# Kernel tuning notes

Hardware: AMD Instinct MI355X
Metric: run time of the kernel (lower is better)

## Reference

```python
import jax, jax.numpy as jnp
import numpy as np

N_NODES = 100000
N_EDGES = 3200000
N_GRAPHS = 2000
F_IN, H, N_CLS = 14, 64, 2


def _glorot(key, shape):
    lim = float(np.sqrt(6.0 / (shape[0] + shape[1])))
    return jax.random.uniform(key, shape, jnp.float32, -lim, lim)


def setup_inputs() -> dict:
    key = jax.random.key(0)
    ks = jax.random.split(key, 16)
    x = jax.random.normal(ks[0], (N_NODES, F_IN), jnp.float32)
    edge_index = jax.random.randint(ks[1], (2, N_EDGES), 0, N_NODES, jnp.int64)
    batch = jnp.sort(jax.random.randint(ks[2], (N_NODES,), 0, N_GRAPHS, jnp.int64))
    return {
        "x": x,
        "W1l": _glorot(ks[3], (F_IN, H)), "W1r": _glorot(ks[4], (F_IN, H)), "b1": jnp.zeros((H,), jnp.float32),
        "W2l": _glorot(ks[5], (H, H)), "W2r": _glorot(ks[6], (H, H)), "b2": jnp.zeros((H,), jnp.float32),
        "W3l": _glorot(ks[7], (H, H)), "W3r": _glorot(ks[8], (H, H)), "b3": jnp.zeros((H,), jnp.float32),
        "W4l": _glorot(ks[9], (H, N_CLS)), "W4r": _glorot(ks[10], (H, N_CLS)), "b4": jnp.zeros((N_CLS,), jnp.float32),
        "edge_index": edge_index,
        "batch": batch,
    }


def _sage_conv(x, Wl, Wr, b, src, dst, inv_deg):
    # mean-aggregate neighbor features: messages flow src -> dst (PyG SAGEConv default)
    agg = jax.ops.segment_sum(x[src], dst, num_segments=N_NODES) * inv_deg
    return agg @ Wl + x @ Wr + b


def reference(x, W1l, W1r, b1, W2l, W2r, b2, W3l, W3r, b3, W4l, W4r, b4, edge_index, batch):
    src, dst = edge_index[0], edge_index[1]
    ones = jnp.ones((src.shape[0],), x.dtype)
    deg = jax.ops.segment_sum(ones, dst, num_segments=N_NODES)
    inv_deg = (1.0 / jnp.maximum(deg, 1.0))[:, None]  # [N,1], isolated nodes -> 0 agg

    h = jax.nn.relu(_sage_conv(x, W1l, W1r, b1, src, dst, inv_deg))
    h = jax.nn.relu(_sage_conv(h, W2l, W2r, b2, src, dst, inv_deg))
    h = jax.nn.relu(_sage_conv(h, W3l, W3r, b3, src, dst, inv_deg))
    h = _sage_conv(h, W4l, W4r, b4, src, dst, inv_deg)

    # global_mean_pool over graphs
    gsum = jax.ops.segment_sum(h, batch, num_segments=N_GRAPHS)
    gcnt = jax.ops.segment_sum(jnp.ones((h.shape[0],), h.dtype), batch, num_segments=N_GRAPHS)
    pooled = gsum / jnp.maximum(gcnt, 1.0)[:, None]
    return jax.nn.log_softmax(pooled, axis=-1)
```

## Files before the change

### kernel.cpp

```cpp
#include <hip/hip_runtime.h>
#include <hip/hip_fp16.h>

#define NN 100000
#define NE 3200000
#define NG 2000
#define FIN 14
#define HD 64
#define NC 2

#define NBUK 256
#define BNODES 391
#define P1E 4096
#define BUFCAP 13312

typedef unsigned int uint;
typedef short short8 __attribute__((ext_vector_type(8)));
typedef float f32x4 __attribute__((ext_vector_type(4)));
union U128 { uint4 u; short8 s; };

__device__ __forceinline__ __half2 u2h(uint u) {
    union { uint u; __half2 h; } c; c.u = u; return c.h;
}
__device__ __forceinline__ uint h2u(__half2 h) {
    union { __half2 h; uint u; } c; c.h = h; return c.u;
}
__device__ __forceinline__ uint pkh(float a, float b) {
    return h2u(__floats2half2_rn(a, b));
}
__device__ __forceinline__ uint pack2bf16(float a, float b) {
    uint ua = __float_as_uint(a), ub = __float_as_uint(b);
    ua = (ua + 0x7FFFu + ((ua >> 16) & 1u)) >> 16;
    ub = (ub + 0x7FFFu + ((ub >> 16) & 1u)) >> 16;
    return ua | (ub << 16);
}
__device__ __forceinline__ short bf16of(float a) {
    uint ua = __float_as_uint(a);
    return (short)((ua + 0x7FFFu + ((ua >> 16) & 1u)) >> 16);
}


__global__ __launch_bounds__(256) void k_hist_bucket(const int* __restrict__ dst,
                                                     int* __restrict__ bkcnt) {
    __shared__ int cnt[NBUK];
    int t = threadIdx.x;
    cnt[t] = 0;
    __syncthreads();
    int e0 = blockIdx.x * P1E;
    int m = NE - e0; if (m > P1E) m = P1E;
    for (int e = t; e < m; e += 256) atomicAdd(&cnt[dst[e0 + e] / BNODES], 1);
    __syncthreads();
    if (cnt[t] > 0) atomicAdd(&bkcnt[t], cnt[t]);
}

__global__ void k_scanb(const int* __restrict__ bkcnt, int* __restrict__ bbase,
                        int* __restrict__ bcur) {
    __shared__ int tmp[NBUK];
    int t = threadIdx.x;
    int v = bkcnt[t];
    tmp[t] = v;
    __syncthreads();
    for (int off = 1; off < NBUK; off <<= 1) {
        int u = (t >= off) ? tmp[t - off] : 0;
        __syncthreads();
        tmp[t] += u;
        __syncthreads();
    }
    int excl = tmp[t] - v;
    bbase[t] = excl;
    bcur[t] = excl;
    if (t == NBUK - 1) bbase[NBUK] = tmp[t];
}

__global__ void k_gbounds(const int* __restrict__ batch, int* __restrict__ gstart,
                          int* __restrict__ gend) {
    int i = blockIdx.x * blockDim.x + threadIdx.x;
    if (i < NN) {
        int b = batch[i];
        if (i == 0 || batch[i - 1] != b) gstart[b] = i;
        if (i == NN - 1 || batch[i + 1] != b) gend[b] = i + 1;
    }
}

__global__ __launch_bounds__(256) void k_pass1(
    const int* __restrict__ src, const int* __restrict__ dst,
    int* __restrict__ bcur, int* __restrict__ pairs) {
    __shared__ int cnt[NBUK];
    __shared__ int scanb[NBUK + 1];
    __shared__ int cur[NBUK];
    __shared__ int gbase[NBUK];
    __shared__ int pbuf[P1E];
    __shared__ unsigned char bsl[P1E];
    int t = threadIdx.x;
    int e0 = blockIdx.x * P1E;
    int m = NE - e0; if (m > P1E) m = P1E;
    cnt[t] = 0;
    __syncthreads();
    int ds[16], ss[16], bk[16];
#pragma unroll
    for (int j = 0; j < 16; ++j) {
        int e = t + j * 256;
        if (e < m) {
            ds[j] = dst[e0 + e];
            ss[j] = src[e0 + e];
            bk[j] = ds[j] / BNODES;
            atomicAdd(&cnt[bk[j]], 1);
        } else bk[j] = -1;
    }
    __syncthreads();
    int v = cnt[t];
    scanb[t] = v;
    __syncthreads();
    for (int off = 1; off < 256; off <<= 1) {
        int u = (t >= off) ? scanb[t - off] : 0;
        __syncthreads();
        scanb[t] += u;
        __syncthreads();
    }
    int excl = scanb[t] - v;
    scanb[t] = excl;
    cur[t] = excl;
    if (t == 255) scanb[256] = excl + v;
    __syncthreads();
#pragma unroll
    for (int j = 0; j < 16; ++j) {
        if (bk[j] >= 0) {
            int p = atomicAdd(&cur[bk[j]], 1);
            pbuf[p] = ss[j] | ((ds[j] - bk[j] * BNODES) << 17);
            bsl[p] = (unsigned char)bk[j];
        }
    }
    int cb = scanb[t + 1] - scanb[t];
    if (cb > 0) gbase[t] = atomicAdd(&bcur[t], cb);
    __syncthreads();
    for (int s = t; s < m; s += 256) {
        int b = bsl[s];
        pairs[gbase[b] + (s - scanb[b])] = pbuf[s];
    }
}

__global__ __launch_bounds__(256) void k_pass2(
    const int* __restrict__ pairs, const int* __restrict__ bbase,
    int* __restrict__ deg, int* __restrict__ rs, int* __restrict__ csr) {
    __shared__ int buf1[BUFCAP];
    __shared__ int buf2[BUFCAP];
    __shared__ int cnt[512];
    __shared__ int rsl[512];
    __shared__ int cur[512];
    __shared__ int s1[256];
    int b = blockIdx.x;
    int n0 = b * BNODES;
    if (n0 >= NN) return;
    int nlocal = NN - n0; if (nlocal > BNODES) nlocal = BNODES;
    int t = threadIdx.x;
    int base = bbase[b];
    int m = bbase[b + 1] - base;
    bool fits = (m <= BUFCAP);
    cnt[t] = 0; cnt[t + 256] = 0;
    __syncthreads();
    for (int s = t; s < m; s += 256) {
        int pk = pairs[base + s];
        if (fits) buf1[s] = pk;
        atomicAdd(&cnt[(uint)pk >> 17], 1);
    }
    __syncthreads();
    int c0 = cnt[2 * t], c1 = cnt[2 * t + 1];
    int ps = c0 + c1;
    s1[t] = ps;
    __syncthreads();
    for (int off = 1; off < 256; off <<= 1) {
        int u = (t >= off) ? s1[t - off] : 0;
        __syncthreads();
        s1[t] += u;
        __syncthreads();
    }
    int pexcl = s1[t] - ps;
    rsl[2 * t] = pexcl;          cur[2 * t] = pexcl;
    rsl[2 * t + 1] = pexcl + c0; cur[2 * t + 1] = pexcl + c0;
    __syncthreads();
    for (int i = t; i < nlocal; i += 256) {
        deg[n0 + i] = cnt[i];
        rs[n0 + i] = base + rsl[i];
    }
    if (fits) {
        for (int s = t; s < m; s += 256) {
            int pk = buf1[s];
            int p = atomicAdd(&cur[(uint)pk >> 17], 1);
            buf2[p] = pk & 0x1FFFF;
        }
        __syncthreads();
        for (int s = t; s < m; s += 256) csr[base + s] = buf2[s];
    } else {
        for (int s = t; s < m; s += 256) {
            int pk = pairs[base + s];
            int p = atomicAdd(&cur[(uint)pk >> 17], 1);
            csr[base + p] = pk & 0x1FFFF;
        }
    }
}


__global__ void k_packx(const float* __restrict__ x, uint* __restrict__ xh) {
    int t = blockIdx.x * blockDim.x + threadIdx.x;
    if (t < NN * 8) {
        int row = t >> 3, q = t & 7;
        int j0 = 2 * q, j1 = 2 * q + 1;
        float f0 = (j0 < FIN) ? x[row * FIN + j0] : 0.f;
        float f1 = (j1 < FIN) ? x[row * FIN + j1] : 0.f;
        xh[t] = pkh(f0, f1);
    }
}


__global__ __launch_bounds__(256, 6) void k_layer1(
    const float* __restrict__ x, const uint* __restrict__ xh, uint* __restrict__ hout,
    const float* __restrict__ Wl, const float* __restrict__ Wr, const float* __restrict__ b,
    const int* __restrict__ rs, const int* __restrict__ deg, const int* __restrict__ csr) {
    __shared__ float2 sW[FIN][HD];
    __shared__ float sb[HD];
    __shared__ float2 sAH[4][16];
    for (int i = threadIdx.x; i < FIN * HD; i += 256) {
        int k = i >> 6, j = i & 63;
        sW[k][j] = make_float2(Wl[i], Wr[i]);
    }
    if (threadIdx.x < HD) sb[threadIdx.x] = b[threadIdx.x];
    __syncthreads();
    int lane = threadIdx.x & 63, wid = threadIdx.x >> 6;
    int sub = lane >> 3;
    int fq = lane & 7;
    int ngroups = (NN + 3) / 4;
    for (int g = blockIdx.x; g < ngroups; g += gridDim.x) {
        int n = g * 4 + wid;
        bool act = n < NN;
        if (act) {
            int s0 = rs[n], d = deg[n];
            float xv = (lane < FIN) ? x[n * FIN + lane] : 0.f;
            __half2 Z = __float2half2_rn(0.f);
            __half2 A0 = Z, A1 = Z, A2 = Z, A3 = Z, A4 = Z, A5 = Z, A6 = Z, A7 = Z;
            for (int base = 0; base < d; base += 64) {
                int rem = d - base; if (rem > 64) rem = 64;
                int idxv = (lane < rem) ? csr[s0 + base + lane] : 0;
                int j = 0;
                for (; j + 64 <= rem; j += 64) {
                    int i0 = __shfl(idxv, j + 0 + sub);
                    int i1 = __shfl(idxv, j + 8 + sub);
                    int i2 = __shfl(idxv, j + 16 + sub);
                    int i3 = __shfl(idxv, j + 24 + sub);
                    int i4 = __shfl(idxv, j + 32 + sub);
                    int i5 = __shfl(idxv, j + 40 + sub);
                    int i6 = __shfl(idxv, j + 48 + sub);
                    int i7 = __shfl(idxv, j + 56 + sub);
                    A0 = __hadd2(A0, u2h(xh[(size_t)i0 * 8 + fq]));
                    A1 = __hadd2(A1, u2h(xh[(size_t)i1 * 8 + fq]));
                    A2 = __hadd2(A2, u2h(xh[(size_t)i2 * 8 + fq]));
                    A3 = __hadd2(A3, u2h(xh[(size_t)i3 * 8 + fq]));
                    A4 = __hadd2(A4, u2h(xh[(size_t)i4 * 8 + fq]));
                    A5 = __hadd2(A5, u2h(xh[(size_t)i5 * 8 + fq]));
                    A6 = __hadd2(A6, u2h(xh[(size_t)i6 * 8 + fq]));
                    A7 = __hadd2(A7, u2h(xh[(size_t)i7 * 8 + fq]));
                }
                for (; j + 8 <= rem; j += 8) {
                    int i0 = __shfl(idxv, j + sub);
                    A0 = __hadd2(A0, u2h(xh[(size_t)i0 * 8 + fq]));
                }
                if (j < rem) {
                    int i0 = __shfl(idxv, j + sub);
                    if (sub < rem - j) A0 = __hadd2(A0, u2h(xh[(size_t)i0 * 8 + fq]));
                }
            }
            A0 = __hadd2(A0, A1); A2 = __hadd2(A2, A3);
            A4 = __hadd2(A4, A5); A6 = __hadd2(A6, A7);
            A0 = __hadd2(A0, A2); A4 = __hadd2(A4, A6);
            A0 = __hadd2(A0, A4);
            float ax = __low2float(A0), ay = __high2float(A0);
            for (int off = 8; off <= 32; off <<= 1) {
                ax += __shfl_xor(ax, off);
                ay += __shfl_xor(ay, off);
            }
            float inv = 1.0f / (float)(d > 1 ? d : 1);
            float e0 = __shfl(ax, lane >> 1);
            float e1 = __shfl(ay, lane >> 1);
            float sel = (lane & 1) ? e1 : e0;
            if (lane < 16) sAH[wid][lane] = make_float2((lane < FIN) ? sel * inv : 0.f, xv);
        }
        float out = sb[lane];
#pragma unroll
        for (int k = 0; k < FIN; ++k) {
            float2 w = sW[k][lane];
            float2 ah = sAH[wid][k];
            out += ah.x * w.x + ah.y * w.y;
        }
        out = fmaxf(out, 0.f);
        float o2 = __shfl_xor(out, 1);
        if (act && !(lane & 1)) hout[(size_t)n * 32 + (lane >> 1)] = pkh(out, o2);
    }
}


template <bool FUSEZ>
__global__ __launch_bounds__(256, 4) void k_layerH(
    const uint* __restrict__ hin, uint* __restrict__ hout,
    const float* __restrict__ Wl, const float* __restrict__ Wr, const float* __restrict__ b,
    const float* __restrict__ W4l, float* __restrict__ z,
    const int* __restrict__ rs, const int* __restrict__ deg, const int* __restrict__ csr) {
    __shared__ uint AH[16 * 64];
    __shared__ float zb[4][16][2];
    int lane = threadIdx.x & 63, wid = threadIdx.x >> 6;
    int r16 = lane & 15, qg = lane >> 4;
    int jj = 16 * wid + r16;
    short8 bfr[4];
#pragma unroll
    for (int c = 0; c < 4; ++c) {
#pragma unroll
        for (int i = 0; i < 8; ++i) {
            int k = 32 * c + 8 * qg + i;
            float v = (k < 64) ? Wl[k * 64 + jj] : Wr[(k - 64) * 64 + jj];
            bfr[c][i] = bf16of(v);
        }
    }
    float bv = b[jj];
    float wz0 = 0.f, wz1 = 0.f;
    if (FUSEZ) { wz0 = W4l[jj * NC + 0]; wz1 = W4l[jj * NC + 1]; }
    int sub = lane >> 4;
    int fq = lane & 15;
    const uint2* hb2 = (const uint2*)hin;
    int n0 = blockIdx.x * 16;
    for (int i = 0; i < 4; ++i) {
        int irow = wid * 4 + i;
        int n = n0 + irow;
        int swz = (irow & 7) << 2;
        if (n < NN) {
            int s0 = rs[n], d = deg[n];
            __half2 Zh = __float2half2_rn(0.f);
            __half2 P0 = Zh, P1 = Zh, P2 = Zh, P3 = Zh, P4 = Zh, P5 = Zh, P6 = Zh, P7 = Zh;
            __half2 Q0 = Zh, Q1 = Zh, Q2 = Zh, Q3 = Zh, Q4 = Zh, Q5 = Zh, Q6 = Zh, Q7 = Zh;
            for (int base = 0; base < d; base += 64) {
                int rem = d - base; if (rem > 64) rem = 64;
                int idxv = (lane < rem) ? csr[s0 + base + lane] : 0;
                int j = 0;
                for (; j + 32 <= rem; j += 32) {
                    int i0 = __shfl(idxv, j + 0 + sub);
                    int i1 = __shfl(idxv, j + 4 + sub);
                    int i2 = __shfl(idxv, j + 8 + sub);
                    int i3 = __shfl(idxv, j + 12 + sub);
                    int i4 = __shfl(idxv, j + 16 + sub);
                    int i5 = __shfl(idxv, j + 20 + sub);
                    int i6 = __shfl(idxv, j + 24 + sub);
                    int i7 = __shfl(idxv, j + 28 + sub);
                    uint2 U;
                    U = hb2[(size_t)i0 * 16 + fq]; P0 = __hadd2(P0, u2h(U.x)); Q0 = __hadd2(Q0, u2h(U.y));
                    U = hb2[(size_t)i1 * 16 + fq]; P1 = __hadd2(P1, u2h(U.x)); Q1 = __hadd2(Q1, u2h(U.y));
                    U = hb2[(size_t)i2 * 16 + fq]; P2 = __hadd2(P2, u2h(U.x)); Q2 = __hadd2(Q2, u2h(U.y));
                    U = hb2[(size_t)i3 * 16 + fq]; P3 = __hadd2(P3, u2h(U.x)); Q3 = __hadd2(Q3, u2h(U.y));
                    U = hb2[(size_t)i4 * 16 + fq]; P4 = __hadd2(P4, u2h(U.x)); Q4 = __hadd2(Q4, u2h(U.y));
                    U = hb2[(size_t)i5 * 16 + fq]; P5 = __hadd2(P5, u2h(U.x)); Q5 = __hadd2(Q5, u2h(U.y));
                    U = hb2[(size_t)i6 * 16 + fq]; P6 = __hadd2(P6, u2h(U.x)); Q6 = __hadd2(Q6, u2h(U.y));
                    U = hb2[(size_t)i7 * 16 + fq]; P7 = __hadd2(P7, u2h(U.x)); Q7 = __hadd2(Q7, u2h(U.y));
                }
                for (; j + 4 <= rem; j += 4) {
                    int i0 = __shfl(idxv, j + sub);
                    uint2 U = hb2[(size_t)i0 * 16 + fq];
                    P0 = __hadd2(P0, u2h(U.x)); Q0 = __hadd2(Q0, u2h(U.y));
                }
                if (j < rem) {
                    int i0 = __shfl(idxv, j + sub);
                    if (sub < rem - j) {
                        uint2 U = hb2[(size_t)i0 * 16 + fq];
                        P0 = __hadd2(P0, u2h(U.x)); Q0 = __hadd2(Q0, u2h(U.y));
                    }
                }
            }
            P0 = __hadd2(P0, P1); P2 = __hadd2(P2, P3);
            P4 = __hadd2(P4, P5); P6 = __hadd2(P6, P7);
            Q0 = __hadd2(Q0, Q1); Q2 = __hadd2(Q2, Q3);
            Q4 = __hadd2(Q4, Q5); Q6 = __hadd2(Q6, Q7);
            P0 = __hadd2(P0, P2); P4 = __hadd2(P4, P6);
            Q0 = __hadd2(Q0, Q2); Q4 = __hadd2(Q4, Q6);
            P0 = __hadd2(P0, P4); Q0 = __hadd2(Q0, Q4);
            float ax = __low2float(P0), ay = __high2float(P0);
            float az = __low2float(Q0), aw = __high2float(Q0);
            for (int off = 16; off <= 32; off <<= 1) {
                ax += __shfl_xor(ax, off);
                ay += __shfl_xor(ay, off);
                az += __shfl_xor(az, off);
                aw += __shfl_xor(aw, off);
            }
            float inv = 1.0f / (float)(d > 1 ? d : 1);
            ax *= inv; ay *= inv; az *= inv; aw *= inv;
            if (lane < 16) {
                uint2* p = (uint2*)&AH[irow * 64 + ((2 * fq) ^ swz)];
                *p = make_uint2(pack2bf16(ax, ay), pack2bf16(az, aw));
            }
            if (lane < 32) {
                __half2 hh = u2h(hin[(size_t)n * 32 + lane]);
                AH[irow * 64 + ((32 + lane) ^ swz)] = pack2bf16(__low2float(hh), __high2float(hh));
            }
        } else {
            AH[irow * 64 + lane] = 0;
        }
    }
    __syncthreads();
    f32x4 acc = (f32x4){bv, bv, bv, bv};
#pragma unroll
    for (int c = 0; c < 4; ++c) {
        U128 a;
        a.u = *(const uint4*)&AH[r16 * 64 + ((16 * c + 4 * qg) ^ ((r16 & 7) << 2))];
        acc = __builtin_amdgcn_mfma_f32_16x16x32_bf16(a.s, bfr[c], acc, 0, 0, 0);
    }
    float rz0[4], rz1[4];
#pragma unroll
    for (int r = 0; r < 4; ++r) {
        int m = n0 + qg * 4 + r;
        float out = fmaxf(acc[r], 0.f);
        float o2 = __shfl_xor(out, 1);
        if (!(lane & 1) && m < NN)
            hout[(size_t)m * 32 + 8 * wid + (r16 >> 1)] = pkh(out, o2);
        if (FUSEZ) { rz0[r] = out * wz0; rz1[r] = out * wz1; }
    }
    if (FUSEZ) {
#pragma unroll
        for (int r = 0; r < 4; ++r) {
            float a0 = rz0[r], a1 = rz1[r];
            for (int off = 1; off < 16; off <<= 1) {
                a0 += __shfl_xor(a0, off);
                a1 += __shfl_xor(a1, off);
            }
            if (r16 == 0) { zb[wid][qg * 4 + r][0] = a0; zb[wid][qg * 4 + r][1] = a1; }
        }
        __syncthreads();
        int t = threadIdx.x;
        if (t < 16 && n0 + t < NN) {
            float a0 = zb[0][t][0] + zb[1][t][0] + zb[2][t][0] + zb[3][t][0];
            float a1 = zb[0][t][1] + zb[1][t][1] + zb[2][t][1] + zb[3][t][1];
            ((float2*)z)[n0 + t] = make_float2(a0, a1);
        }
    }
}


__global__ __launch_bounds__(256) void k_pool(
    const uint* __restrict__ h3, const float* __restrict__ z,
    const float* __restrict__ W4r, const float* __restrict__ b4,
    const int* __restrict__ rs, const int* __restrict__ deg, const int* __restrict__ csr,
    const int* __restrict__ batch, float* __restrict__ gsum) {
    __shared__ float sW[HD * NC];
    if (threadIdx.x < HD * NC) sW[threadIdx.x] = W4r[threadIdx.x];
    __syncthreads();
    const float2* z2 = (const float2*)z;
    int lane = threadIdx.x & 63, wid = threadIdx.x >> 6;
    int stride = gridDim.x * 4;
    for (int n = blockIdx.x * 4 + wid; n < NN; n += stride) {
        float r0 = 0.f, r1 = 0.f;
        if (lane < 32) {
            __half2 h = u2h(h3[(size_t)n * 32 + lane]);
            float f0 = __low2float(h), f1 = __high2float(h);
            r0 = f0 * sW[(2 * lane) * NC + 0] + f1 * sW[(2 * lane + 1) * NC + 0];
            r1 = f0 * sW[(2 * lane) * NC + 1] + f1 * sW[(2 * lane + 1) * NC + 1];
        }
        int s0 = rs[n], d = deg[n];
        float a0 = 0.f, a1 = 0.f;
        for (int j = lane; j < d; j += 64) {
            int s = csr[s0 + j];
            float2 zv = z2[s];
            a0 += zv.x;
            a1 += zv.y;
        }
        for (int off = 32; off; off >>= 1) {
            r0 += __shfl_xor(r0, off);
            r1 += __shfl_xor(r1, off);
            a0 += __shfl_xor(a0, off);
            a1 += __shfl_xor(a1, off);
        }
        if (lane == 0) {
            float inv = 1.0f / (float)(d > 1 ? d : 1);
            float o0 = a0 * inv + r0 + b4[0];
            float o1 = a1 * inv + r1 + b4[1];
            int gg = batch[n];
            atomicAdd(&gsum[gg * 2 + 0], o0);
            atomicAdd(&gsum[gg * 2 + 1], o1);
        }
    }
}

__global__ void k_final(const float* __restrict__ gsum, const int* __restrict__ gstart,
                        const int* __restrict__ gend, float* __restrict__ out) {
    int g = blockIdx.x * blockDim.x + threadIdx.x;
    if (g < NG) {
        int cnt = gend[g] - gstart[g];
        float inv = 1.0f / (float)(cnt > 1 ? cnt : 1);
        float p0 = gsum[g * 2 + 0] * inv;
        float p1 = gsum[g * 2 + 1] * inv;
        float m = fmaxf(p0, p1);
        float lse = m + logf(expf(p0 - m) + expf(p1 - m));
        out[g * 2 + 0] = p0 - lse;
        out[g * 2 + 1] = p1 - lse;
    }
}


extern "C" void kernel_launch(void* const* d_in, const int* in_sizes, int n_in,
                              void* d_out, int out_size, void* d_ws, size_t ws_size,
                              hipStream_t stream) {
    const float* x   = (const float*)d_in[0];
    const float* W1l = (const float*)d_in[1];
    const float* W1r = (const float*)d_in[2];
    const float* b1  = (const float*)d_in[3];
    const float* W2l = (const float*)d_in[4];
    const float* W2r = (const float*)d_in[5];
    const float* b2  = (const float*)d_in[6];
    const float* W3l = (const float*)d_in[7];
    const float* W3r = (const float*)d_in[8];
    const float* b3  = (const float*)d_in[9];
    const float* W4l = (const float*)d_in[10];
    const float* W4r = (const float*)d_in[11];
    const float* b4  = (const float*)d_in[12];
    const int* ei    = (const int*)d_in[13];
    const int* batch = (const int*)d_in[14];
    const int* src = ei;
    const int* dst = ei + NE;
    float* out = (float*)d_out;

    char* w = (char*)d_ws;
    int* deg    = (int*)w; w += (size_t)NN * 4;
    int* rs     = (int*)w; w += (size_t)NN * 4;
    int* csr    = (int*)w; w += (size_t)NE * 4;
    int* gstart = (int*)w; w += (size_t)NG * 4;
    int* gend   = (int*)w; w += (size_t)NG * 4;
    int* bkcnt  = (int*)w; w += NBUK * 4;
    int* bbase  = (int*)w; w += (NBUK + 1) * 4;
    int* bcur   = (int*)w; w += NBUK * 4;
    w = (char*)(((uintptr_t)w + 255) & ~(uintptr_t)255);
    uint* xh    = (uint*)w; w += (size_t)NN * 8 * 4;
    uint* hA    = (uint*)w; w += (size_t)NN * 32 * 4;
    uint* hB    = (uint*)w; w += (size_t)NN * 32 * 4;
    float* z    = (float*)w; w += (size_t)NN * NC * 4;
    float* gsum = (float*)w; w += (size_t)NG * NC * 4;
    int* pairs = (int*)hB;

    const int P1B = (NE + P1E - 1) / P1E;
    const int HGB = (NN + 15) / 16;

    hipMemsetAsync(bkcnt, 0, NBUK * 4, stream);
    hipMemsetAsync(gstart, 0, (size_t)NG * 4, stream);
    hipMemsetAsync(gend, 0, (size_t)NG * 4, stream);
    hipMemsetAsync(gsum, 0, (size_t)NG * NC * 4, stream);

    k_hist_bucket<<<P1B, 256, 0, stream>>>(dst, bkcnt);
    k_packx<<<(NN * 8 + 255) / 256, 256, 0, stream>>>(x, xh);
    k_gbounds<<<(NN + 255) / 256, 256, 0, stream>>>(batch, gstart, gend);
    k_scanb<<<1, NBUK, 0, stream>>>(bkcnt, bbase, bcur);
    k_pass1<<<P1B, 256, 0, stream>>>(src, dst, bcur, pairs);
    k_pass2<<<NBUK, 256, 0, stream>>>(pairs, bbase, deg, rs, csr);

    k_layer1<<<1536, 256, 0, stream>>>(x, xh, hA, W1l, W1r, b1, rs, deg, csr);
    k_layerH<false><<<HGB, 256, 0, stream>>>(hA, hB, W2l, W2r, b2, nullptr, nullptr, rs, deg, csr);
    k_layerH<true><<<HGB, 256, 0, stream>>>(hB, hA, W3l, W3r, b3, W4l, z, rs, deg, csr);
    k_pool<<<2048, 256, 0, stream>>>(hA, z, W4r, b4, rs, deg, csr, batch, gsum);
    k_final<<<(NG + 255) / 256, 256, 0, stream>>>(gsum, gstart, gend, out);
}
```

Baseline: 424.3 us.

## Load CSR indices directly per lane, reduce in half2, fuse root projection into layer3

```diff
diff --git a/kernel.cpp b/kernel.cpp
--- a/kernel.cpp
+++ b/kernel.cpp
@@ -36,6 +36,9 @@
 __device__ __forceinline__ short bf16of(float a) {
     uint ua = __float_as_uint(a);
     return (short)((ua + 0x7FFFu + ((ua >> 16) & 1u)) >> 16);
+}
+__device__ __forceinline__ __half2 hredx(__half2 v, int off) {
+    return __hadd2(v, u2h((uint)__shfl_xor((int)h2u(v), off)));
 }
 
 
@@ -225,57 +228,53 @@
     if (threadIdx.x < HD) sb[threadIdx.x] = b[threadIdx.x];
     __syncthreads();
     int lane = threadIdx.x & 63, wid = threadIdx.x >> 6;
-    int sub = lane >> 3;
-    int fq = lane & 7;
+    int sub8 = lane >> 3;
+    int fq8 = lane & 7;
     int ngroups = (NN + 3) / 4;
     for (int g = blockIdx.x; g < ngroups; g += gridDim.x) {
         int n = g * 4 + wid;
         bool act = n < NN;
         if (act) {
             int s0 = rs[n], d = deg[n];
+            const int* cp = csr + s0;
             float xv = (lane < FIN) ? x[n * FIN + lane] : 0.f;
             __half2 Z = __float2half2_rn(0.f);
             __half2 A0 = Z, A1 = Z, A2 = Z, A3 = Z, A4 = Z, A5 = Z, A6 = Z, A7 = Z;
-            for (int base = 0; base < d; base += 64) {
-                int rem = d - base; if (rem > 64) rem = 64;
-                int idxv = (lane < rem) ? csr[s0 + base + lane] : 0;
-                int j = 0;
-                for (; j + 64 <= rem; j += 64) {
-                    int i0 = __shfl(idxv, j + 0 + sub);
-                    int i1 = __shfl(idxv, j + 8 + sub);
-                    int i2 = __shfl(idxv, j + 16 + sub);
-                    int i3 = __shfl(idxv, j + 24 + sub);
-                    int i4 = __shfl(idxv, j + 32 + sub);
-                    int i5 = __shfl(idxv, j + 40 + sub);
-                    int i6 = __shfl(idxv, j + 48 + sub);
-                    int i7 = __shfl(idxv, j + 56 + sub);
-                    A0 = __hadd2(A0, u2h(xh[(size_t)i0 * 8 + fq]));
-                    A1 = __hadd2(A1, u2h(xh[(size_t)i1 * 8 + fq]));
-                    A2 = __hadd2(A2, u2h(xh[(size_t)i2 * 8 + fq]));
-                    A3 = __hadd2(A3, u2h(xh[(size_t)i3 * 8 + fq]));
-                    A4 = __hadd2(A4, u2h(xh[(size_t)i4 * 8 + fq]));
-                    A5 = __hadd2(A5, u2h(xh[(size_t)i5 * 8 + fq]));
-                    A6 = __hadd2(A6, u2h(xh[(size_t)i6 * 8 + fq]));
-                    A7 = __hadd2(A7, u2h(xh[(size_t)i7 * 8 + fq]));
-                }
-                for (; j + 8 <= rem; j += 8) {
-                    int i0 = __shfl(idxv, j + sub);
-                    A0 = __hadd2(A0, u2h(xh[(size_t)i0 * 8 + fq]));
-                }
-                if (j < rem) {
-                    int i0 = __shfl(idxv, j + sub);
-                    if (sub < rem - j) A0 = __hadd2(A0, u2h(xh[(size_t)i0 * 8 + fq]));
-                }
+            int e = 0;
+            for (; e + 64 <= d; e += 64) {
+                int i0 = cp[e + 0 + sub8];
+                int i1 = cp[e + 8 + sub8];
+                int i2 = cp[e + 16 + sub8];
+                int i3 = cp[e + 24 + sub8];
+                int i4 = cp[e + 32 + sub8];
+                int i5 = cp[e + 40 + sub8];
+                int i6 = cp[e + 48 + sub8];
+                int i7 = cp[e + 56 + sub8];
+                A0 = __hadd2(A0, u2h(xh[(size_t)i0 * 8 + fq8]));
+                A1 = __hadd2(A1, u2h(xh[(size_t)i1 * 8 + fq8]));
+                A2 = __hadd2(A2, u2h(xh[(size_t)i2 * 8 + fq8]));
+                A3 = __hadd2(A3, u2h(xh[(size_t)i3 * 8 + fq8]));
+                A4 = __hadd2(A4, u2h(xh[(size_t)i4 * 8 + fq8]));
+                A5 = __hadd2(A5, u2h(xh[(size_t)i5 * 8 + fq8]));
+                A6 = __hadd2(A6, u2h(xh[(size_t)i6 * 8 + fq8]));
+                A7 = __hadd2(A7, u2h(xh[(size_t)i7 * 8 + fq8]));
+            }
+            for (; e + 8 <= d; e += 8) {
+                int i0 = cp[e + sub8];
+                A0 = __hadd2(A0, u2h(xh[(size_t)i0 * 8 + fq8]));
+            }
+            if (e < d) {
+                int ei = e + sub8;
+                int i0 = cp[ei < d ? ei : d - 1];
+                uint u = xh[(size_t)i0 * 8 + fq8];
+                if (ei < d) A0 = __hadd2(A0, u2h(u));
             }
             A0 = __hadd2(A0, A1); A2 = __hadd2(A2, A3);
             A4 = __hadd2(A4, A5); A6 = __hadd2(A6, A7);
             A0 = __hadd2(A0, A2); A4 = __hadd2(A4, A6);
             A0 = __hadd2(A0, A4);
+            A0 = hredx(A0, 8); A0 = hredx(A0, 16); A0 = hredx(A0, 32);
             float ax = __low2float(A0), ay = __high2float(A0);
-            for (int off = 8; off <= 32; off <<= 1) {
-                ax += __shfl_xor(ax, off);
-                ay += __shfl_xor(ay, off);
-            }
             float inv = 1.0f / (float)(d > 1 ? d : 1);
             float e0 = __shfl(ax, lane >> 1);
             float e1 = __shfl(ay, lane >> 1);
@@ -300,10 +299,11 @@
 __global__ __launch_bounds__(256, 4) void k_layerH(
     const uint* __restrict__ hin, uint* __restrict__ hout,
     const float* __restrict__ Wl, const float* __restrict__ Wr, const float* __restrict__ b,
-    const float* __restrict__ W4l, float* __restrict__ z,
+    const float* __restrict__ W4l, const float* __restrict__ W4r, const float* __restrict__ b4g,
+    float* __restrict__ z, float* __restrict__ s2,
     const int* __restrict__ rs, const int* __restrict__ deg, const int* __restrict__ csr) {
     __shared__ uint AH[16 * 64];
-    __shared__ float zb[4][16][2];
+    __shared__ float zb[4][16][4];
     int lane = threadIdx.x & 63, wid = threadIdx.x >> 6;
     int r16 = lane & 15, qg = lane >> 4;
     int jj = 16 * wid + r16;
@@ -318,9 +318,12 @@
         }
     }
     float bv = b[jj];
-    float wz0 = 0.f, wz1 = 0.f;
-    if (FUSEZ) { wz0 = W4l[jj * NC + 0]; wz1 = W4l[jj * NC + 1]; }
-    int sub = lane >> 4;
+    float wz0 = 0.f, wz1 = 0.f, ws0 = 0.f, ws1 = 0.f;
+    if (FUSEZ) {
+        wz0 = W4l[jj * NC + 0]; wz1 = W4l[jj * NC + 1];
+        ws0 = W4r[jj * NC + 0]; ws1 = W4r[jj * NC + 1];
+    }
+    int sub4 = lane >> 4;
     int fq = lane & 15;
     const uint2* hb2 = (const uint2*)hin;
     int n0 = blockIdx.x * 16;
@@ -330,44 +333,40 @@
         int swz = (irow & 7) << 2;
         if (n < NN) {
             int s0 = rs[n], d = deg[n];
+            const int* cp = csr + s0;
             __half2 Zh = __float2half2_rn(0.f);
             __half2 P0 = Zh, P1 = Zh, P2 = Zh, P3 = Zh, P4 = Zh, P5 = Zh, P6 = Zh, P7 = Zh;
             __half2 Q0 = Zh, Q1 = Zh, Q2 = Zh, Q3 = Zh, Q4 = Zh, Q5 = Zh, Q6 = Zh, Q7 = Zh;
-            for (int base = 0; base < d; base += 64) {
-                int rem = d - base; if (rem > 64) rem = 64;
-                int idxv = (lane < rem) ? csr[s0 + base + lane] : 0;
-                int j = 0;
-                for (; j + 32 <= rem; j += 32) {
-                    int i0 = __shfl(idxv, j + 0 + sub);
-                    int i1 = __shfl(idxv, j + 4 + sub);
-                    int i2 = __shfl(idxv, j + 8 + sub);
-                    int i3 = __shfl(idxv, j + 12 + sub);
-                    int i4 = __shfl(idxv, j + 16 + sub);
-                    int i5 = __shfl(idxv, j + 20 + sub);
-                    int i6 = __shfl(idxv, j + 24 + sub);
-                    int i7 = __shfl(idxv, j + 28 + sub);
-                    uint2 U;
-                    U = hb2[(size_t)i0 * 16 + fq]; P0 = __hadd2(P0, u2h(U.x)); Q0 = __hadd2(Q0, u2h(U.y));
-                    U = hb2[(size_t)i1 * 16 + fq]; P1 = __hadd2(P1, u2h(U.x)); Q1 = __hadd2(Q1, u2h(U.y));
-                    U = hb2[(size_t)i2 * 16 + fq]; P2 = __hadd2(P2, u2h(U.x)); Q2 = __hadd2(Q2, u2h(U.y));
-                    U = hb2[(size_t)i3 * 16 + fq]; P3 = __hadd2(P3, u2h(U.x)); Q3 = __hadd2(Q3, u2h(U.y));
-                    U = hb2[(size_t)i4 * 16 + fq]; P4 = __hadd2(P4, u2h(U.x)); Q4 = __hadd2(Q4, u2h(U.y));
-                    U = hb2[(size_t)i5 * 16 + fq]; P5 = __hadd2(P5, u2h(U.x)); Q5 = __hadd2(Q5, u2h(U.y));
-                    U = hb2[(size_t)i6 * 16 + fq]; P6 = __hadd2(P6, u2h(U.x)); Q6 = __hadd2(Q6, u2h(U.y));
-                    U = hb2[(size_t)i7 * 16 + fq]; P7 = __hadd2(P7, u2h(U.x)); Q7 = __hadd2(Q7, u2h(U.y));
-                }
-                for (; j + 4 <= rem; j += 4) {
-                    int i0 = __shfl(idxv, j + sub);
-                    uint2 U = hb2[(size_t)i0 * 16 + fq];
-                    P0 = __hadd2(P0, u2h(U.x)); Q0 = __hadd2(Q0, u2h(U.y));
-                }
-                if (j < rem) {
-                    int i0 = __shfl(idxv, j + sub);
-                    if (sub < rem - j) {
-                        uint2 U = hb2[(size_t)i0 * 16 + fq];
-                        P0 = __hadd2(P0, u2h(U.x)); Q0 = __hadd2(Q0, u2h(U.y));
-                    }
-                }
+            int e = 0;
+            for (; e + 32 <= d; e += 32) {
+                int i0 = cp[e + 0 + sub4];
+                int i1 = cp[e + 4 + sub4];
+                int i2 = cp[e + 8 + sub4];
+                int i3 = cp[e + 12 + sub4];
+                int i4 = cp[e + 16 + sub4];
+                int i5 = cp[e + 20 + sub4];
+                int i6 = cp[e + 24 + sub4];
+                int i7 = cp[e + 28 + sub4];
+                uint2 U;
+                U = hb2[(size_t)i0 * 16 + fq]; P0 = __hadd2(P0, u2h(U.x)); Q0 = __hadd2(Q0, u2h(U.y));
+                U = hb2[(size_t)i1 * 16 + fq]; P1 = __hadd2(P1, u2h(U.x)); Q1 = __hadd2(Q1, u2h(U.y));
+                U = hb2[(size_t)i2 * 16 + fq]; P2 = __hadd2(P2, u2h(U.x)); Q2 = __hadd2(Q2, u2h(U.y));
+                U = hb2[(size_t)i3 * 16 + fq]; P3 = __hadd2(P3, u2h(U.x)); Q3 = __hadd2(Q3, u2h(U.y));
+                U = hb2[(size_t)i4 * 16 + fq]; P4 = __hadd2(P4, u2h(U.x)); Q4 = __hadd2(Q4, u2h(U.y));
+                U = hb2[(size_t)i5 * 16 + fq]; P5 = __hadd2(P5, u2h(U.x)); Q5 = __hadd2(Q5, u2h(U.y));
+                U = hb2[(size_t)i6 * 16 + fq]; P6 = __hadd2(P6, u2h(U.x)); Q6 = __hadd2(Q6, u2h(U.y));
+                U = hb2[(size_t)i7 * 16 + fq]; P7 = __hadd2(P7, u2h(U.x)); Q7 = __hadd2(Q7, u2h(U.y));
+            }
+            for (; e + 4 <= d; e += 4) {
+                int i0 = cp[e + sub4];
+                uint2 U = hb2[(size_t)i0 * 16 + fq];
+                P0 = __hadd2(P0, u2h(U.x)); Q0 = __hadd2(Q0, u2h(U.y));
+            }
+            if (e < d) {
+                int ei = e + sub4;
+                int i0 = cp[ei < d ? ei : d - 1];
+                uint2 U = hb2[(size_t)i0 * 16 + fq];
+                if (ei < d) { P0 = __hadd2(P0, u2h(U.x)); Q0 = __hadd2(Q0, u2h(U.y)); }
             }
             P0 = __hadd2(P0, P1); P2 = __hadd2(P2, P3);
             P4 = __hadd2(P4, P5); P6 = __hadd2(P6, P7);
@@ -376,17 +375,12 @@
             P0 = __hadd2(P0, P2); P4 = __hadd2(P4, P6);
             Q0 = __hadd2(Q0, Q2); Q4 = __hadd2(Q4, Q6);
             P0 = __hadd2(P0, P4); Q0 = __hadd2(Q0, Q4);
-            float ax = __low2float(P0), ay = __high2float(P0);
-            float az = __low2float(Q0), aw = __high2float(Q0);
-            for (int off = 16; off <= 32; off <<= 1) {
-                ax += __shfl_xor(ax, off);
-                ay += __shfl_xor(ay, off);
-                az += __shfl_xor(az, off);
-                aw += __shfl_xor(aw, off);
-            }
+            P0 = hredx(P0, 16); P0 = hredx(P0, 32);
+            Q0 = hredx(Q0, 16); Q0 = hredx(Q0, 32);
             float inv = 1.0f / (float)(d > 1 ? d : 1);
-            ax *= inv; ay *= inv; az *= inv; aw *= inv;
             if (lane < 16) {
+                float ax = __low2float(P0) * inv, ay = __high2float(P0) * inv;
+                float az = __low2float(Q0) * inv, aw = __high2float(Q0) * inv;
                 uint2* p = (uint2*)&AH[irow * 64 + ((2 * fq) ^ swz)];
                 *p = make_uint2(pack2bf16(ax, ay), pack2bf16(az, aw));
             }
@@ -406,7 +400,7 @@
         a.u = *(const uint4*)&AH[r16 * 64 + ((16 * c + 4 * qg) ^ ((r16 & 7) << 2))];
         acc = __builtin_amdgcn_mfma_f32_16x16x32_bf16(a.s, bfr[c], acc, 0, 0, 0);
     }
-    float rz0[4], rz1[4];
+    float rz0[4], rz1[4], rs0[4], rs1[4];
 #pragma unroll
     for (int r = 0; r < 4; ++r) {
         int m = n0 + qg * 4 + r;
@@ -414,48 +408,49 @@
         float o2 = __shfl_xor(out, 1);
         if (!(lane & 1) && m < NN)
             hout[(size_t)m * 32 + 8 * wid + (r16 >> 1)] = pkh(out, o2);
-        if (FUSEZ) { rz0[r] = out * wz0; rz1[r] = out * wz1; }
+        if (FUSEZ) {
+            rz0[r] = out * wz0; rz1[r] = out * wz1;
+            rs0[r] = out * ws0; rs1[r] = out * ws1;
+        }
     }
     if (FUSEZ) {
 #pragma unroll
         for (int r = 0; r < 4; ++r) {
-            float a0 = rz0[r], a1 = rz1[r];
+            float a0 = rz0[r], a1 = rz1[r], b0 = rs0[r], b1 = rs1[r];
             for (int off = 1; off < 16; off <<= 1) {
                 a0 += __shfl_xor(a0, off);
                 a1 += __shfl_xor(a1, off);
-            }
-            if (r16 == 0) { zb[wid][qg * 4 + r][0] = a0; zb[wid][qg * 4 + r][1] = a1; }
+                b0 += __shfl_xor(b0, off);
+                b1 += __shfl_xor(b1, off);
+            }
+            if (r16 == 0) {
+                zb[wid][qg * 4 + r][0] = a0; zb[wid][qg * 4 + r][1] = a1;
+                zb[wid][qg * 4 + r][2] = b0; zb[wid][qg * 4 + r][3] = b1;
+            }
         }
         __syncthreads();
         int t = threadIdx.x;
         if (t < 16 && n0 + t < NN) {
             float a0 = zb[0][t][0] + zb[1][t][0] + zb[2][t][0] + zb[3][t][0];
             float a1 = zb[0][t][1] + zb[1][t][1] + zb[2][t][1] + zb[3][t][1];
+            float c0 = zb[0][t][2] + zb[1][t][2] + zb[2][t][2] + zb[3][t][2];
+            float c1 = zb[0][t][3] + zb[1][t][3] + zb[2][t][3] + zb[3][t][3];
             ((float2*)z)[n0 + t] = make_float2(a0, a1);
+            ((float2*)s2)[n0 + t] = make_float2(c0 + b4g[0], c1 + b4g[1]);
         }
     }
 }
 
 
 __global__ __launch_bounds__(256) void k_pool(
-    const uint* __restrict__ h3, const float* __restrict__ z,
-    const float* __restrict__ W4r, const float* __restrict__ b4,
+    const float* __restrict__ z, const float* __restrict__ s2,
     const int* __restrict__ rs, const int* __restrict__ deg, const int* __restrict__ csr,
     const int* __restrict__ batch, float* __restrict__ gsum) {
-    __shared__ float sW[HD * NC];
-    if (threadIdx.x < HD * NC) sW[threadIdx.x] = W4r[threadIdx.x];
-    __syncthreads();
     const float2* z2 = (const float2*)z;
+    const float2* s22 = (const float2*)s2;
     int lane = threadIdx.x & 63, wid = threadIdx.x >> 6;
     int stride = gridDim.x * 4;
     for (int n = blockIdx.x * 4 + wid; n < NN; n += stride) {
-        float r0 = 0.f, r1 = 0.f;
-        if (lane < 32) {
-            __half2 h = u2h(h3[(size_t)n * 32 + lane]);
-            float f0 = __low2float(h), f1 = __high2float(h);
-            r0 = f0 * sW[(2 * lane) * NC + 0] + f1 * sW[(2 * lane + 1) * NC + 0];
-            r1 = f0 * sW[(2 * lane) * NC + 1] + f1 * sW[(2 * lane + 1) * NC + 1];
-        }
         int s0 = rs[n], d = deg[n];
         float a0 = 0.f, a1 = 0.f;
         for (int j = lane; j < d; j += 64) {
@@ -465,15 +460,14 @@
             a1 += zv.y;
         }
         for (int off = 32; off; off >>= 1) {
-            r0 += __shfl_xor(r0, off);
-            r1 += __shfl_xor(r1, off);
             a0 += __shfl_xor(a0, off);
             a1 += __shfl_xor(a1, off);
         }
         if (lane == 0) {
+            float2 sv = s22[n];
             float inv = 1.0f / (float)(d > 1 ? d : 1);
-            float o0 = a0 * inv + r0 + b4[0];
-            float o1 = a1 * inv + r1 + b4[1];
+            float o0 = a0 * inv + sv.x;
+            float o1 = a1 * inv + sv.y;
             int gg = batch[n];
             atomicAdd(&gsum[gg * 2 + 0], o0);
             atomicAdd(&gsum[gg * 2 + 1], o1);
@@ -533,6 +527,7 @@
     uint* hA    = (uint*)w; w += (size_t)NN * 32 * 4;
     uint* hB    = (uint*)w; w += (size_t)NN * 32 * 4;
     float* z    = (float*)w; w += (size_t)NN * NC * 4;
+    float* s2   = (float*)w; w += (size_t)NN * NC * 4;
     float* gsum = (float*)w; w += (size_t)NG * NC * 4;
     int* pairs = (int*)hB;
 
@@ -552,8 +547,12 @@
     k_pass2<<<NBUK, 256, 0, stream>>>(pairs, bbase, deg, rs, csr);
 
     k_layer1<<<1536, 256, 0, stream>>>(x, xh, hA, W1l, W1r, b1, rs, deg, csr);
-    k_layerH<false><<<HGB, 256, 0, stream>>>(hA, hB, W2l, W2r, b2, nullptr, nullptr, rs, deg, csr);
-    k_layerH<true><<<HGB, 256, 0, stream>>>(hB, hA, W3l, W3r, b3, W4l, z, rs, deg, csr);
-    k_pool<<<2048, 256, 0, stream>>>(hA, z, W4r, b4, rs, deg, csr, batch, gsum);
+    k_layerH<false><<<HGB, 256, 0, stream>>>(hA, hB, W2l, W2r, b2,
+                                             nullptr, nullptr, nullptr, nullptr, nullptr,
+                                             rs, deg, csr);
+    k_layerH<true><<<HGB, 256, 0, stream>>>(hB, hA, W3l, W3r, b3,
+                                            W4l, W4r, b4, z, s2,
+                                            rs, deg, csr);
+    k_pool<<<2048, 256, 0, stream>>>(z, s2, rs, deg, csr, batch, gsum);
     k_final<<<(NG + 255) / 256, 256, 0, stream>>>(gsum, gstart, gend, out);
 }
```

After: 456.8 us. 1.08x slower.

## Fuse layer-4 root projection into layer-3 epilogue, halve shuffle reductions, raise occupancy

Applied to the files above, without the earlier changes.

```diff
diff --git a/kernel.cpp b/kernel.cpp
--- a/kernel.cpp
+++ b/kernel.cpp
@@ -36,6 +36,9 @@
 __device__ __forceinline__ short bf16of(float a) {
     uint ua = __float_as_uint(a);
     return (short)((ua + 0x7FFFu + ((ua >> 16) & 1u)) >> 16);
+}
+__device__ __forceinline__ __half2 hredx(__half2 v, int off) {
+    return __hadd2(v, u2h((uint)__shfl_xor((int)h2u(v), off)));
 }
 
 
@@ -271,11 +274,8 @@
             A4 = __hadd2(A4, A5); A6 = __hadd2(A6, A7);
             A0 = __hadd2(A0, A2); A4 = __hadd2(A4, A6);
             A0 = __hadd2(A0, A4);
+            A0 = hredx(A0, 8); A0 = hredx(A0, 16); A0 = hredx(A0, 32);
             float ax = __low2float(A0), ay = __high2float(A0);
-            for (int off = 8; off <= 32; off <<= 1) {
-                ax += __shfl_xor(ax, off);
-                ay += __shfl_xor(ay, off);
-            }
             float inv = 1.0f / (float)(d > 1 ? d : 1);
             float e0 = __shfl(ax, lane >> 1);
             float e1 = __shfl(ay, lane >> 1);
@@ -297,13 +297,14 @@
 
 
 template <bool FUSEZ>
-__global__ __launch_bounds__(256, 4) void k_layerH(
+__global__ __launch_bounds__(256, 8) void k_layerH(
     const uint* __restrict__ hin, uint* __restrict__ hout,
     const float* __restrict__ Wl, const float* __restrict__ Wr, const float* __restrict__ b,
-    const float* __restrict__ W4l, float* __restrict__ z,
+    const float* __restrict__ W4l, const float* __restrict__ W4r, const float* __restrict__ b4g,
+    float* __restrict__ z, float* __restrict__ s2,
     const int* __restrict__ rs, const int* __restrict__ deg, const int* __restrict__ csr) {
     __shared__ uint AH[16 * 64];
-    __shared__ float zb[4][16][2];
+    __shared__ float zb[4][16][4];
     int lane = threadIdx.x & 63, wid = threadIdx.x >> 6;
     int r16 = lane & 15, qg = lane >> 4;
     int jj = 16 * wid + r16;
@@ -318,8 +319,11 @@
         }
     }
     float bv = b[jj];
-    float wz0 = 0.f, wz1 = 0.f;
-    if (FUSEZ) { wz0 = W4l[jj * NC + 0]; wz1 = W4l[jj * NC + 1]; }
+    float wz0 = 0.f, wz1 = 0.f, ws0 = 0.f, ws1 = 0.f;
+    if (FUSEZ) {
+        wz0 = W4l[jj * NC + 0]; wz1 = W4l[jj * NC + 1];
+        ws0 = W4r[jj * NC + 0]; ws1 = W4r[jj * NC + 1];
+    }
     int sub = lane >> 4;
     int fq = lane & 15;
     const uint2* hb2 = (const uint2*)hin;
@@ -376,17 +380,12 @@
             P0 = __hadd2(P0, P2); P4 = __hadd2(P4, P6);
             Q0 = __hadd2(Q0, Q2); Q4 = __hadd2(Q4, Q6);
             P0 = __hadd2(P0, P4); Q0 = __hadd2(Q0, Q4);
-            float ax = __low2float(P0), ay = __high2float(P0);
-            float az = __low2float(Q0), aw = __high2float(Q0);
-            for (int off = 16; off <= 32; off <<= 1) {
-                ax += __shfl_xor(ax, off);
-                ay += __shfl_xor(ay, off);
-                az += __shfl_xor(az, off);
-                aw += __shfl_xor(aw, off);
-            }
+            P0 = hredx(P0, 16); P0 = hredx(P0, 32);
+            Q0 = hredx(Q0, 16); Q0 = hredx(Q0, 32);
             float inv = 1.0f / (float)(d > 1 ? d : 1);
-            ax *= inv; ay *= inv; az *= inv; aw *= inv;
             if (lane < 16) {
+                float ax = __low2float(P0) * inv, ay = __high2float(P0) * inv;
+                float az = __low2float(Q0) * inv, aw = __high2float(Q0) * inv;
                 uint2* p = (uint2*)&AH[irow * 64 + ((2 * fq) ^ swz)];
                 *p = make_uint2(pack2bf16(ax, ay), pack2bf16(az, aw));
             }
@@ -406,7 +405,7 @@
         a.u = *(const uint4*)&AH[r16 * 64 + ((16 * c + 4 * qg) ^ ((r16 & 7) << 2))];
         acc = __builtin_amdgcn_mfma_f32_16x16x32_bf16(a.s, bfr[c], acc, 0, 0, 0);
     }
-    float rz0[4], rz1[4];
+    float rz0[4], rz1[4], rs0[4], rs1[4];
 #pragma unroll
     for (int r = 0; r < 4; ++r) {
         int m = n0 + qg * 4 + r;
@@ -414,48 +413,49 @@
         float o2 = __shfl_xor(out, 1);
         if (!(lane & 1) && m < NN)
             hout[(size_t)m * 32 + 8 * wid + (r16 >> 1)] = pkh(out, o2);
-        if (FUSEZ) { rz0[r] = out * wz0; rz1[r] = out * wz1; }
+        if (FUSEZ) {
+            rz0[r] = out * wz0; rz1[r] = out * wz1;
+            rs0[r] = out * ws0; rs1[r] = out * ws1;
+        }
     }
     if (FUSEZ) {
 #pragma unroll
         for (int r = 0; r < 4; ++r) {
-            float a0 = rz0[r], a1 = rz1[r];
+            float a0 = rz0[r], a1 = rz1[r], b0 = rs0[r], b1 = rs1[r];
             for (int off = 1; off < 16; off <<= 1) {
                 a0 += __shfl_xor(a0, off);
                 a1 += __shfl_xor(a1, off);
+                b0 += __shfl_xor(b0, off);
+                b1 += __shfl_xor(b1, off);
             }
-            if (r16 == 0) { zb[wid][qg * 4 + r][0] = a0; zb[wid][qg * 4 + r][1] = a1; }
+            if (r16 == 0) {
+                zb[wid][qg * 4 + r][0] = a0; zb[wid][qg * 4 + r][1] = a1;
+                zb[wid][qg * 4 + r][2] = b0; zb[wid][qg * 4 + r][3] = b1;
+            }
         }
         __syncthreads();
         int t = threadIdx.x;
         if (t < 16 && n0 + t < NN) {
             float a0 = zb[0][t][0] + zb[1][t][0] + zb[2][t][0] + zb[3][t][0];
             float a1 = zb[0][t][1] + zb[1][t][1] + zb[2][t][1] + zb[3][t][1];
+            float c0 = zb[0][t][2] + zb[1][t][2] + zb[2][t][2] + zb[3][t][2];
+            float c1 = zb[0][t][3] + zb[1][t][3] + zb[2][t][3] + zb[3][t][3];
             ((float2*)z)[n0 + t] = make_float2(a0, a1);
+            ((float2*)s2)[n0 + t] = make_float2(c0 + b4g[0], c1 + b4g[1]);
         }
     }
 }
 
 
 __global__ __launch_bounds__(256) void k_pool(
-    const uint* __restrict__ h3, const float* __restrict__ z,
-    const float* __restrict__ W4r, const float* __restrict__ b4,
+    const float* __restrict__ z, const float* __restrict__ s2,
     const int* __restrict__ rs, const int* __restrict__ deg, const int* __restrict__ csr,
     const int* __restrict__ batch, float* __restrict__ gsum) {
-    __shared__ float sW[HD * NC];
-    if (threadIdx.x < HD * NC) sW[threadIdx.x] = W4r[threadIdx.x];
-    __syncthreads();
     const float2* z2 = (const float2*)z;
+    const float2* s22 = (const float2*)s2;
     int lane = threadIdx.x & 63, wid = threadIdx.x >> 6;
     int stride = gridDim.x * 4;
     for (int n = blockIdx.x * 4 + wid; n < NN; n += stride) {
-        float r0 = 0.f, r1 = 0.f;
-        if (lane < 32) {
-            __half2 h = u2h(h3[(size_t)n * 32 + lane]);
-            float f0 = __low2float(h), f1 = __high2float(h);
-            r0 = f0 * sW[(2 * lane) * NC + 0] + f1 * sW[(2 * lane + 1) * NC + 0];
-            r1 = f0 * sW[(2 * lane) * NC + 1] + f1 * sW[(2 * lane + 1) * NC + 1];
-        }
         int s0 = rs[n], d = deg[n];
         float a0 = 0.f, a1 = 0.f;
         for (int j = lane; j < d; j += 64) {
@@ -465,15 +465,14 @@
             a1 += zv.y;
         }
         for (int off = 32; off; off >>= 1) {
-            r0 += __shfl_xor(r0, off);
-            r1 += __shfl_xor(r1, off);
             a0 += __shfl_xor(a0, off);
             a1 += __shfl_xor(a1, off);
         }
         if (lane == 0) {
+            float2 sv = s22[n];
             float inv = 1.0f / (float)(d > 1 ? d : 1);
-            float o0 = a0 * inv + r0 + b4[0];
-            float o1 = a1 * inv + r1 + b4[1];
+            float o0 = a0 * inv + sv.x;
+            float o1 = a1 * inv + sv.y;
             int gg = batch[n];
             atomicAdd(&gsum[gg * 2 + 0], o0);
             atomicAdd(&gsum[gg * 2 + 1], o1);
@@ -533,6 +532,7 @@
     uint* hA    = (uint*)w; w += (size_t)NN * 32 * 4;
     uint* hB    = (uint*)w; w += (size_t)NN * 32 * 4;
     float* z    = (float*)w; w += (size_t)NN * NC * 4;
+    float* s2   = (float*)w; w += (size_t)NN * NC * 4;
     float* gsum = (float*)w; w += (size_t)NG * NC * 4;
     int* pairs = (int*)hB;
 
@@ -552,8 +552,12 @@
     k_pass2<<<NBUK, 256, 0, stream>>>(pairs, bbase, deg, rs, csr);
 
     k_layer1<<<1536, 256, 0, stream>>>(x, xh, hA, W1l, W1r, b1, rs, deg, csr);
-    k_layerH<false><<<HGB, 256, 0, stream>>>(hA, hB, W2l, W2r, b2, nullptr, nullptr, rs, deg, csr);
-    k_layerH<true><<<HGB, 256, 0, stream>>>(hB, hA, W3l, W3r, b3, W4l, z, rs, deg, csr);
-    k_pool<<<2048, 256, 0, stream>>>(hA, z, W4r, b4, rs, deg, csr, batch, gsum);
+    k_layerH<false><<<HGB, 256, 0, stream>>>(hA, hB, W2l, W2r, b2,
+                                             nullptr, nullptr, nullptr, nullptr, nullptr,
+                                             rs, deg, csr);
+    k_layerH<true><<<HGB, 256, 0, stream>>>(hB, hA, W3l, W3r, b3,
+                                            W4l, W4r, b4, z, s2,
+                                            rs, deg, csr);
+    k_pool<<<2048, 256, 0, stream>>>(z, s2, rs, deg, csr, batch, gsum);
     k_final<<<(NG + 255) / 256, 256, 0, stream>>>(gsum, gstart, gend, out);
 }
```

Measured after the change: 481.8 us. +13.5%, slower.
